# Optimization experiments

Measured on AMD Instinct MI355X. Metric: run time of the kernel, lower is better.

The kernel has to match this reference:

```python
import jax, jax.numpy as jnp
import numpy as np
import math

N_EMBD = 1024
N_HEAD = 16
HEAD_DIM = N_EMBD // N_HEAD
SCALE = 1.0 / math.sqrt(HEAD_DIM)


def setup_inputs() -> dict:
    key = jax.random.key(0)
    ks = jax.random.split(key, 5)
    B, S = 1, 4096
    std = 0.02
    x = jax.random.normal(ks[0], (B, S, N_EMBD), dtype=jnp.float32)
    # Linear weights stored as [in, out] (transposed vs torch storage; same math)
    w_qkv = jax.random.normal(ks[1], (N_EMBD, 3 * N_EMBD), dtype=jnp.float32) * std
    b_qkv = jnp.zeros((3 * N_EMBD,), dtype=jnp.float32)
    w_out = jax.random.normal(ks[2], (N_EMBD, N_EMBD), dtype=jnp.float32) * std
    b_out = jnp.zeros((N_EMBD,), dtype=jnp.float32)
    return {"x": x, "w_qkv": w_qkv, "b_qkv": b_qkv, "w_out": w_out, "b_out": b_out}


def reference(x, w_qkv, b_qkv, w_out, b_out):
    B, S, D = x.shape
    qkv = x @ w_qkv + b_qkv                      # [B, S, 3D]
    q, k, v = jnp.split(qkv, 3, axis=-1)
    # [B, H, S, d]
    q = q.reshape(B, S, N_HEAD, HEAD_DIM).transpose(0, 2, 1, 3)
    k = k.reshape(B, S, N_HEAD, HEAD_DIM).transpose(0, 2, 1, 3)
    v = v.reshape(B, S, N_HEAD, HEAD_DIM).transpose(0, 2, 1, 3)
    scores = jnp.einsum("bhqd,bhkd->bhqk", q, k) * SCALE  # [B, H, S, S]
    causal = jnp.tril(jnp.ones((S, S), dtype=bool))
    scores = jnp.where(causal, scores, -jnp.inf)
    attn = jax.nn.softmax(scores, axis=-1)
    out = jnp.einsum("bhqk,bhkd->bhqd", attn, v)  # [B, H, S, d]
    out = out.transpose(0, 2, 1, 3).reshape(B, S, D)
    return out @ w_out + b_out
```

## Files before the change

### kernel.cpp

```cpp
#include <hip/hip_runtime.h>
#include <hip/hip_bf16.h>
#include <cstdint>

typedef __bf16 bf16x8 __attribute__((ext_vector_type(8)));
typedef float  f32x4  __attribute__((ext_vector_type(4)));

#define S_LEN 4096
#define D_EMB 1024
#define N3    3072
#define HDIM  64

__device__ __forceinline__ unsigned short f2bf(float f) {
    union { unsigned int i; float f; } v; v.f = f;
    unsigned int i = v.i;
    return (unsigned short)((i + 0x7FFFu + ((i >> 16) & 1u)) >> 16);
}

__device__ __forceinline__ void async16(const void* g, void* l) {
    __builtin_amdgcn_global_load_lds(
        (const __attribute__((address_space(1))) unsigned int*)g,
        (__attribute__((address_space(3))) unsigned int*)l,
        16, 0, 0);
}

__global__ void convert_f32_bf16(const float* __restrict__ src,
                                 unsigned short* __restrict__ dst, int n8) {
    const int i = blockIdx.x * blockDim.x + threadIdx.x;
    if (i >= n8) return;
    float4 f0 = *(const float4*)&src[i * 8];
    float4 f1 = *(const float4*)&src[i * 8 + 4];
    union { uint4 q; unsigned short s[8]; } o;
    o.s[0]=f2bf(f0.x); o.s[1]=f2bf(f0.y); o.s[2]=f2bf(f0.z); o.s[3]=f2bf(f0.w);
    o.s[4]=f2bf(f1.x); o.s[5]=f2bf(f1.y); o.s[6]=f2bf(f1.z); o.s[7]=f2bf(f1.w);
    *(uint4*)&dst[i * 8] = o.q;
}

__global__ void transpose_f32_to_bf16(const float* __restrict__ src,
                                      unsigned short* __restrict__ dst,
                                      int R, int ld, int c0) {
    __shared__ float tile[32][33];
    const int tx = threadIdx.x, ty = threadIdx.y;
    const int r0 = blockIdx.y * 32, cc0 = blockIdx.x * 32;
    for (int i = 0; i < 32; i += 8)
        tile[ty + i][tx] = src[(size_t)(r0 + ty + i) * ld + c0 + cc0 + tx];
    __syncthreads();
    for (int i = 0; i < 32; i += 8)
        dst[(size_t)(cc0 + ty + i) * R + r0 + tx] = f2bf(tile[tx][ty + i]);
}

__global__ void transpose_bf16(const unsigned short* __restrict__ src,
                               unsigned short* __restrict__ dst,
                               int R, int ld, int c0) {
    __shared__ unsigned short tile[32][33];
    const int tx = threadIdx.x, ty = threadIdx.y;
    const int r0 = blockIdx.y * 32, cc0 = blockIdx.x * 32;
    for (int i = 0; i < 32; i += 8)
        tile[ty + i][tx] = src[(size_t)(r0 + ty + i) * ld + c0 + cc0 + tx];
    __syncthreads();
    for (int i = 0; i < 32; i += 8)
        dst[(size_t)(cc0 + ty + i) * R + r0 + tx] = tile[tx][ty + i];
}

template <bool OUT_F32>
__global__ __launch_bounds__(256) void gemm_bt_bias(
    const unsigned short* __restrict__ A,
    const unsigned short* __restrict__ BT,
    const float* __restrict__ bias,
    void* __restrict__ Cp,
    int M, int N, int K)
{
    __shared__ __align__(16) unsigned short As[128 * 32];
    __shared__ __align__(16) unsigned short Bs[128 * 32];
    const int tid  = threadIdx.x;
    const int wave = tid >> 6, lane = tid & 63;
    const int q4 = lane >> 4, l16 = lane & 15;
    const int m0 = blockIdx.y * 128, n0 = blockIdx.x * 128;
    const int wm = (wave >> 1) * 64, wn = (wave & 1) * 64;

    f32x4 acc[4][4] = {};

    const int srow = wave * 32 + (lane >> 2);
    const int scol = (lane & 3) * 8;

    for (int k0 = 0; k0 < K; k0 += 32) {
        __syncthreads();
        for (int i = 0; i < 2; ++i) {
            const int r = srow + i * 16;
            async16(A  + (size_t)(m0 + r) * K + k0 + scol,
                    &As[(wave * 32 + i * 16) * 32 + lane * 8]);
            async16(BT + (size_t)(n0 + r) * K + k0 + scol,
                    &Bs[(wave * 32 + i * 16) * 32 + lane * 8]);
        }
        __syncthreads();

        bf16x8 af[4], bfr[4];
        for (int mi = 0; mi < 4; ++mi)
            af[mi] = *(const bf16x8*)&As[(wm + mi * 16 + l16) * 32 + q4 * 8];
        for (int ni = 0; ni < 4; ++ni)
            bfr[ni] = *(const bf16x8*)&Bs[(wn + ni * 16 + l16) * 32 + q4 * 8];
        for (int mi = 0; mi < 4; ++mi)
            for (int ni = 0; ni < 4; ++ni)
                acc[mi][ni] = __builtin_amdgcn_mfma_f32_16x16x32_bf16(
                    af[mi], bfr[ni], acc[mi][ni], 0, 0, 0);
    }

    for (int ni = 0; ni < 4; ++ni) {
        const int col = n0 + wn + ni * 16 + l16;
        const float bv = bias[col];
        for (int mi = 0; mi < 4; ++mi) {
            const int row = m0 + wm + mi * 16 + q4 * 4;
            for (int r = 0; r < 4; ++r) {
                const float val = acc[mi][ni][r] + bv;
                if constexpr (OUT_F32)
                    ((float*)Cp)[(size_t)(row + r) * N + col] = val;
                else
                    ((unsigned short*)Cp)[(size_t)(row + r) * N + col] = f2bf(val);
            }
        }
    }
}

#define LDP 72
__global__ __launch_bounds__(256) void attn_flash(
    const unsigned short* __restrict__ qkv,
    const unsigned short* __restrict__ Vt,
    unsigned short* __restrict__ X2)
{
    __shared__ __align__(16) unsigned short Ks[64 * LDP];
    __shared__ __align__(16) unsigned short Vs[64 * LDP];
    __shared__ __align__(16) unsigned short Ps[4 * 16 * LDP];
    const int tid  = threadIdx.x;
    const int wave = tid >> 6, lane = tid & 63;
    const int q4 = lane >> 4, l16 = lane & 15;
    const int h  = blockIdx.y;

    const int x = blockIdx.x, hg = blockIdx.y >> 2;
    int qt;
    if      (hg == 0) qt = x;
    else if (hg == 1) qt = 63 - x;
    else if (hg == 2) qt = (x + 16) & 63;
    else              qt = (47 - x) & 63;
    const int q0 = qt * 64;

    bf16x8 aq[2];
    {
        const unsigned short* qp =
            qkv + (size_t)(q0 + wave * 16 + l16) * N3 + h * HDIM + q4 * 8;
        aq[0] = *(const bf16x8*)(qp);
        aq[1] = *(const bf16x8*)(qp + 32);
    }

    float l_part = 0.f;
    f32x4 o[4] = {};

    const int rr = tid >> 3;
    const int cc = (tid & 7) * 8;
    const int ntile = qt + 1;
    const int grow = q0 + wave * 16 + l16;

    uint4 kv_a, kv_b, vt_a, vt_b;
    {
        kv_a = *(const uint4*)&qkv[(size_t)(rr)      * N3 + D_EMB + h * HDIM + cc];
        kv_b = *(const uint4*)&qkv[(size_t)(32 + rr) * N3 + D_EMB + h * HDIM + cc];
        vt_a = *(const uint4*)&Vt [(size_t)(h * HDIM + rr)      * S_LEN + cc];
        vt_b = *(const uint4*)&Vt [(size_t)(h * HDIM + 32 + rr) * S_LEN + cc];
    }

    for (int t = 0; t < ntile; ++t) {
        const int kv0 = t * 64;
        __syncthreads();
        *(uint4*)&Ks[rr * LDP + cc]        = kv_a;
        *(uint4*)&Ks[(32 + rr) * LDP + cc] = kv_b;
        *(uint4*)&Vs[rr * LDP + cc]        = vt_a;
        *(uint4*)&Vs[(32 + rr) * LDP + cc] = vt_b;
        if (t + 1 < ntile) {
            const int kn = kv0 + 64;
            kv_a = *(const uint4*)&qkv[(size_t)(kn + rr)      * N3 + D_EMB + h * HDIM + cc];
            kv_b = *(const uint4*)&qkv[(size_t)(kn + 32 + rr) * N3 + D_EMB + h * HDIM + cc];
            vt_a = *(const uint4*)&Vt [(size_t)(h * HDIM + rr)      * S_LEN + kn + cc];
            vt_b = *(const uint4*)&Vt [(size_t)(h * HDIM + 32 + rr) * S_LEN + kn + cc];
        }
        __syncthreads();

        f32x4 sacc[4] = {};
#pragma unroll
        for (int kk = 0; kk < 2; ++kk)
#pragma unroll
            for (int nt = 0; nt < 4; ++nt) {
                bf16x8 kf = *(const bf16x8*)&Ks[(nt * 16 + l16) * LDP + kk * 32 + q4 * 8];
                sacc[nt] = __builtin_amdgcn_mfma_f32_16x16x32_bf16(
                    kf, aq[kk], sacc[nt], 0, 0, 0);
            }

        bf16x8 vb[2][4];
#pragma unroll
        for (int kk = 0; kk < 2; ++kk)
#pragma unroll
            for (int dt = 0; dt < 4; ++dt)
                vb[kk][dt] = *(const bf16x8*)&Vs[(dt * 16 + l16) * LDP + kk * 32 + q4 * 8];

        const bool lastt = (t == ntile - 1);
#pragma unroll
        for (int nt = 0; nt < 4; ++nt) {
            float e[4];
#pragma unroll
            for (int r = 0; r < 4; ++r) {
                e[r] = __expf(sacc[nt][r] * 0.125f);
                if (lastt && (kv0 + nt * 16 + q4 * 4 + r > grow)) e[r] = 0.f;
                l_part += e[r];
            }
            union { uint2 q; unsigned short w[4]; } pk;
            pk.w[0] = f2bf(e[0]); pk.w[1] = f2bf(e[1]);
            pk.w[2] = f2bf(e[2]); pk.w[3] = f2bf(e[3]);
            *(uint2*)&Ps[wave * 16 * LDP + l16 * LDP + nt * 16 + q4 * 4] = pk.q;
        }
        __asm__ volatile("s_waitcnt lgkmcnt(0)" ::: "memory");

#pragma unroll
        for (int kk = 0; kk < 2; ++kk) {
            bf16x8 pa = *(const bf16x8*)&Ps[wave * 16 * LDP + l16 * LDP + kk * 32 + q4 * 8];
#pragma unroll
            for (int dt = 0; dt < 4; ++dt)
                o[dt] = __builtin_amdgcn_mfma_f32_16x16x32_bf16(
                    pa, vb[kk][dt], o[dt], 0, 0, 0);
        }
    }

    float l = l_part;
    l += __shfl_xor(l, 16);
    l += __shfl_xor(l, 32);
    float linv[4];
#pragma unroll
    for (int r = 0; r < 4; ++r)
        linv[r] = 1.f / __shfl(l, q4 * 4 + r);

#pragma unroll
    for (int dt = 0; dt < 4; ++dt)
#pragma unroll
        for (int r = 0; r < 4; ++r) {
            const int row = q0 + wave * 16 + q4 * 4 + r;
            X2[(size_t)row * D_EMB + h * HDIM + dt * 16 + l16] =
                f2bf(o[dt][r] * linv[r]);
        }
}

extern "C" void kernel_launch(void* const* d_in, const int* in_sizes, int n_in,
                              void* d_out, int out_size, void* d_ws, size_t ws_size,
                              hipStream_t stream) {
    const float* x     = (const float*)d_in[0];
    const float* w_qkv = (const float*)d_in[1];
    const float* b_qkv = (const float*)d_in[2];
    const float* w_out = (const float*)d_in[3];
    const float* b_out = (const float*)d_in[4];
    float* out = (float*)d_out;

    char* ws = (char*)d_ws;
    unsigned short* qkv   = (unsigned short*)(ws);
    unsigned short* wqkvT = (unsigned short*)(ws + 25165824);
    unsigned short* woutT = (unsigned short*)(ws + 31457280);
    unsigned short* Vt    = (unsigned short*)(ws + 33554432);
    unsigned short* X2    = (unsigned short*)(ws + 41943040);
    unsigned short* Xb    = X2;

    convert_f32_bf16<<<(4096 * 1024 / 8 + 255) / 256, 256, 0, stream>>>(
        x, Xb, 4096 * 1024 / 8);

    transpose_f32_to_bf16<<<dim3(3072 / 32, 1024 / 32), dim3(32, 8), 0, stream>>>(
        w_qkv, wqkvT, 1024, 3072, 0);
    transpose_f32_to_bf16<<<dim3(1024 / 32, 1024 / 32), dim3(32, 8), 0, stream>>>(
        w_out, woutT, 1024, 1024, 0);

    gemm_bt_bias<false><<<dim3(3072 / 128, 4096 / 128), 256, 0, stream>>>(
        Xb, wqkvT, b_qkv, qkv, 4096, 3072, 1024);

    transpose_bf16<<<dim3(1024 / 32, 4096 / 32), dim3(32, 8), 0, stream>>>(
        qkv, Vt, 4096, 3072, 2048);

    attn_flash<<<dim3(64, 16), 256, 0, stream>>>(qkv, Vt, X2);

    gemm_bt_bias<true><<<dim3(1024 / 128, 4096 / 128), 256, 0, stream>>>(
        X2, woutT, b_out, out, 4096, 1024, 1024);
}
```

Before: 257.9 us.

## Load K fragments directly from global memory and swizzle GEMM block order

The attention kernel stops staging K tiles through shared memory. Each wave now loads its K MFMA fragments straight from global memory, relying on L2/L1 reuse across the four waves, which removes the LDS writes and reads for K. V staging is kept, but V fragments are now read from LDS just before each PV MFMA instead of being preloaded into registers. Separately, the GEMM kernel remaps block indices with an 8-way swizzle to improve L2 locality. The risk is higher global-load latency exposed in the QK stage, since the K loads are no longer prefetched a tile ahead.

```diff
diff --git a/kernel.cpp b/kernel.cpp
--- a/kernel.cpp
+++ b/kernel.cpp
@@ -74,7 +74,11 @@
     const int tid  = threadIdx.x;
     const int wave = tid >> 6, lane = tid & 63;
     const int q4 = lane >> 4, l16 = lane & 15;
-    const int m0 = blockIdx.y * 128, n0 = blockIdx.x * 128;
+
+    const int nwg = gridDim.x * gridDim.y;
+    const int p   = blockIdx.y * gridDim.x + blockIdx.x;
+    const int swz = (p & 7) * (nwg >> 3) + (p >> 3);
+    const int m0 = (swz / gridDim.x) * 128, n0 = (swz % gridDim.x) * 128;
     const int wm = (wave >> 1) * 64, wn = (wave & 1) * 64;
 
     f32x4 acc[4][4] = {};
@@ -126,7 +130,6 @@
     const unsigned short* __restrict__ Vt,
     unsigned short* __restrict__ X2)
 {
-    __shared__ __align__(16) unsigned short Ks[64 * LDP];
     __shared__ __align__(16) unsigned short Vs[64 * LDP];
     __shared__ __align__(16) unsigned short Ps[4 * 16 * LDP];
     const int tid  = threadIdx.x;
@@ -158,46 +161,50 @@
     const int ntile = qt + 1;
     const int grow = q0 + wave * 16 + l16;
 
-    uint4 kv_a, kv_b, vt_a, vt_b;
+    const unsigned short* kfp =
+        qkv + (size_t)l16 * N3 + D_EMB + h * HDIM + q4 * 8;
+
+    uint4 vt_a, vt_b;
     {
-        kv_a = *(const uint4*)&qkv[(size_t)(rr)      * N3 + D_EMB + h * HDIM + cc];
-        kv_b = *(const uint4*)&qkv[(size_t)(32 + rr) * N3 + D_EMB + h * HDIM + cc];
-        vt_a = *(const uint4*)&Vt [(size_t)(h * HDIM + rr)      * S_LEN + cc];
-        vt_b = *(const uint4*)&Vt [(size_t)(h * HDIM + 32 + rr) * S_LEN + cc];
+        vt_a = *(const uint4*)&Vt[(size_t)(h * HDIM + rr)      * S_LEN + cc];
+        vt_b = *(const uint4*)&Vt[(size_t)(h * HDIM + 32 + rr) * S_LEN + cc];
     }
 
     for (int t = 0; t < ntile; ++t) {
         const int kv0 = t * 64;
         __syncthreads();
-        *(uint4*)&Ks[rr * LDP + cc]        = kv_a;
-        *(uint4*)&Ks[(32 + rr) * LDP + cc] = kv_b;
         *(uint4*)&Vs[rr * LDP + cc]        = vt_a;
         *(uint4*)&Vs[(32 + rr) * LDP + cc] = vt_b;
+        __syncthreads();
+
+        f32x4 sacc[4] = {};
+        const unsigned short* kp = kfp + (size_t)kv0 * N3;
+        {
+            bf16x8 kf[4];
+#pragma unroll
+            for (int nt = 0; nt < 4; ++nt)
+                kf[nt] = *(const bf16x8*)(kp + (size_t)nt * 16 * N3);
+#pragma unroll
+            for (int nt = 0; nt < 4; ++nt)
+                sacc[nt] = __builtin_amdgcn_mfma_f32_16x16x32_bf16(
+                    kf[nt], aq[0], sacc[nt], 0, 0, 0);
+        }
+        {
+            bf16x8 kf[4];
+#pragma unroll
+            for (int nt = 0; nt < 4; ++nt)
+                kf[nt] = *(const bf16x8*)(kp + (size_t)nt * 16 * N3 + 32);
+#pragma unroll
+            for (int nt = 0; nt < 4; ++nt)
+                sacc[nt] = __builtin_amdgcn_mfma_f32_16x16x32_bf16(
+                    kf[nt], aq[1], sacc[nt], 0, 0, 0);
+        }
+
         if (t + 1 < ntile) {
             const int kn = kv0 + 64;
-            kv_a = *(const uint4*)&qkv[(size_t)(kn + rr)      * N3 + D_EMB + h * HDIM + cc];
-            kv_b = *(const uint4*)&qkv[(size_t)(kn + 32 + rr) * N3 + D_EMB + h * HDIM + cc];
-            vt_a = *(const uint4*)&Vt [(size_t)(h * HDIM + rr)      * S_LEN + kn + cc];
-            vt_b = *(const uint4*)&Vt [(size_t)(h * HDIM + 32 + rr) * S_LEN + kn + cc];
-        }
-        __syncthreads();
-
-        f32x4 sacc[4] = {};
-#pragma unroll
-        for (int kk = 0; kk < 2; ++kk)
-#pragma unroll
-            for (int nt = 0; nt < 4; ++nt) {
-                bf16x8 kf = *(const bf16x8*)&Ks[(nt * 16 + l16) * LDP + kk * 32 + q4 * 8];
-                sacc[nt] = __builtin_amdgcn_mfma_f32_16x16x32_bf16(
-                    kf, aq[kk], sacc[nt], 0, 0, 0);
-            }
-
-        bf16x8 vb[2][4];
-#pragma unroll
-        for (int kk = 0; kk < 2; ++kk)
-#pragma unroll
-            for (int dt = 0; dt < 4; ++dt)
-                vb[kk][dt] = *(const bf16x8*)&Vs[(dt * 16 + l16) * LDP + kk * 32 + q4 * 8];
+            vt_a = *(const uint4*)&Vt[(size_t)(h * HDIM + rr)      * S_LEN + kn + cc];
+            vt_b = *(const uint4*)&Vt[(size_t)(h * HDIM + 32 + rr) * S_LEN + kn + cc];
+        }
 
         const bool lastt = (t == ntile - 1);
 #pragma unroll
@@ -220,9 +227,11 @@
         for (int kk = 0; kk < 2; ++kk) {
             bf16x8 pa = *(const bf16x8*)&Ps[wave * 16 * LDP + l16 * LDP + kk * 32 + q4 * 8];
 #pragma unroll
-            for (int dt = 0; dt < 4; ++dt)
+            for (int dt = 0; dt < 4; ++dt) {
+                bf16x8 vb = *(const bf16x8*)&Vs[(dt * 16 + l16) * LDP + kk * 32 + q4 * 8];
                 o[dt] = __builtin_amdgcn_mfma_f32_16x16x32_bf16(
-                    pa, vb[kk][dt], o[dt], 0, 0, 0);
+                    pa, vb, o[dt], 0, 0, 0);
+            }
         }
     }
 
```

New measurement: 300.1 us. +16.4%, slower.

## Deepen GEMM K-step to 64, template BM, and stream V fragments in attention

Applied to the files above, without the earlier changes.

The GEMM now stages a 64-wide K slice per barrier pair (two 32-wide LDS buffers), which halves the number of synchronizations per output tile. It is also templated on BM so the output projection uses 64-row tiles, doubling its grid from 256 to 512 blocks to fill more CUs. In the attention kernel, V fragments are loaded from LDS just before each MFMA instead of all up front, which lowers register pressure. The trade-offs are more LDS per block and lower arithmetic intensity on the smaller tiles.

```diff
diff --git a/kernel.cpp b/kernel.cpp
--- a/kernel.cpp
+++ b/kernel.cpp
@@ -61,7 +61,7 @@
         dst[(size_t)(cc0 + ty + i) * R + r0 + tx] = tile[tx][ty + i];
 }
 
-template <bool OUT_F32>
+template <bool OUT_F32, int BM>
 __global__ __launch_bounds__(256) void gemm_bt_bias(
     const unsigned short* __restrict__ A,
     const unsigned short* __restrict__ BT,
@@ -69,46 +69,66 @@
     void* __restrict__ Cp,
     int M, int N, int K)
 {
-    __shared__ __align__(16) unsigned short As[128 * 32];
-    __shared__ __align__(16) unsigned short Bs[128 * 32];
+    constexpr int MI = BM / 32;
+    __shared__ __align__(16) unsigned short As[2][BM * 32];
+    __shared__ __align__(16) unsigned short Bs[2][128 * 32];
     const int tid  = threadIdx.x;
     const int wave = tid >> 6, lane = tid & 63;
     const int q4 = lane >> 4, l16 = lane & 15;
-    const int m0 = blockIdx.y * 128, n0 = blockIdx.x * 128;
-    const int wm = (wave >> 1) * 64, wn = (wave & 1) * 64;
-
-    f32x4 acc[4][4] = {};
-
-    const int srow = wave * 32 + (lane >> 2);
-    const int scol = (lane & 3) * 8;
-
-    for (int k0 = 0; k0 < K; k0 += 32) {
-        __syncthreads();
-        for (int i = 0; i < 2; ++i) {
-            const int r = srow + i * 16;
-            async16(A  + (size_t)(m0 + r) * K + k0 + scol,
-                    &As[(wave * 32 + i * 16) * 32 + lane * 8]);
-            async16(BT + (size_t)(n0 + r) * K + k0 + scol,
-                    &Bs[(wave * 32 + i * 16) * 32 + lane * 8]);
-        }
-        __syncthreads();
-
-        bf16x8 af[4], bfr[4];
-        for (int mi = 0; mi < 4; ++mi)
-            af[mi] = *(const bf16x8*)&As[(wm + mi * 16 + l16) * 32 + q4 * 8];
-        for (int ni = 0; ni < 4; ++ni)
-            bfr[ni] = *(const bf16x8*)&Bs[(wn + ni * 16 + l16) * 32 + q4 * 8];
-        for (int mi = 0; mi < 4; ++mi)
+    const int m0 = blockIdx.y * BM, n0 = blockIdx.x * 128;
+    const int wm = (wave >> 1) * (BM / 2), wn = (wave & 1) * 64;
+
+    f32x4 acc[MI][4] = {};
+
+    const int srowA = wave * (BM / 4) + (lane >> 2);
+    const int srowB = wave * 32 + (lane >> 2);
+    const int scol  = (lane & 3) * 8;
+
+    for (int k0 = 0; k0 < K; k0 += 64) {
+        __syncthreads();
+#pragma unroll
+        for (int kk = 0; kk < 2; ++kk) {
+#pragma unroll
+            for (int i = 0; i < BM / 64; ++i) {
+                const int r = srowA + i * 16;
+                async16(A + (size_t)(m0 + r) * K + k0 + kk * 32 + scol,
+                        &As[kk][(wave * (BM / 4) + i * 16) * 32 + lane * 8]);
+            }
+#pragma unroll
+            for (int i = 0; i < 2; ++i) {
+                const int r = srowB + i * 16;
+                async16(BT + (size_t)(n0 + r) * K + k0 + kk * 32 + scol,
+                        &Bs[kk][(wave * 32 + i * 16) * 32 + lane * 8]);
+            }
+        }
+        __syncthreads();
+
+#pragma unroll
+        for (int kk = 0; kk < 2; ++kk) {
+            bf16x8 af[MI], bfr[4];
+#pragma unroll
+            for (int mi = 0; mi < MI; ++mi)
+                af[mi] = *(const bf16x8*)&As[kk][(wm + mi * 16 + l16) * 32 + q4 * 8];
+#pragma unroll
             for (int ni = 0; ni < 4; ++ni)
-                acc[mi][ni] = __builtin_amdgcn_mfma_f32_16x16x32_bf16(
-                    af[mi], bfr[ni], acc[mi][ni], 0, 0, 0);
-    }
-
+                bfr[ni] = *(const bf16x8*)&Bs[kk][(wn + ni * 16 + l16) * 32 + q4 * 8];
+#pragma unroll
+            for (int mi = 0; mi < MI; ++mi)
+#pragma unroll
+                for (int ni = 0; ni < 4; ++ni)
+                    acc[mi][ni] = __builtin_amdgcn_mfma_f32_16x16x32_bf16(
+                        af[mi], bfr[ni], acc[mi][ni], 0, 0, 0);
+        }
+    }
+
+#pragma unroll
     for (int ni = 0; ni < 4; ++ni) {
         const int col = n0 + wn + ni * 16 + l16;
         const float bv = bias[col];
-        for (int mi = 0; mi < 4; ++mi) {
+#pragma unroll
+        for (int mi = 0; mi < MI; ++mi) {
             const int row = m0 + wm + mi * 16 + q4 * 4;
+#pragma unroll
             for (int r = 0; r < 4; ++r) {
                 const float val = acc[mi][ni][r] + bv;
                 if constexpr (OUT_F32)
@@ -192,13 +212,6 @@
                     kf, aq[kk], sacc[nt], 0, 0, 0);
             }
 
-        bf16x8 vb[2][4];
-#pragma unroll
-        for (int kk = 0; kk < 2; ++kk)
-#pragma unroll
-            for (int dt = 0; dt < 4; ++dt)
-                vb[kk][dt] = *(const bf16x8*)&Vs[(dt * 16 + l16) * LDP + kk * 32 + q4 * 8];
-
         const bool lastt = (t == ntile - 1);
 #pragma unroll
         for (int nt = 0; nt < 4; ++nt) {
@@ -220,9 +233,11 @@
         for (int kk = 0; kk < 2; ++kk) {
             bf16x8 pa = *(const bf16x8*)&Ps[wave * 16 * LDP + l16 * LDP + kk * 32 + q4 * 8];
 #pragma unroll
-            for (int dt = 0; dt < 4; ++dt)
+            for (int dt = 0; dt < 4; ++dt) {
+                bf16x8 vb = *(const bf16x8*)&Vs[(dt * 16 + l16) * LDP + kk * 32 + q4 * 8];
                 o[dt] = __builtin_amdgcn_mfma_f32_16x16x32_bf16(
-                    pa, vb[kk][dt], o[dt], 0, 0, 0);
+                    pa, vb, o[dt], 0, 0, 0);
+            }
         }
     }
 
@@ -270,7 +285,7 @@
     transpose_f32_to_bf16<<<dim3(1024 / 32, 1024 / 32), dim3(32, 8), 0, stream>>>(
         w_out, woutT, 1024, 1024, 0);
 
-    gemm_bt_bias<false><<<dim3(3072 / 128, 4096 / 128), 256, 0, stream>>>(
+    gemm_bt_bias<false, 128><<<dim3(3072 / 128, 4096 / 128), 256, 0, stream>>>(
         Xb, wqkvT, b_qkv, qkv, 4096, 3072, 1024);
 
     transpose_bf16<<<dim3(1024 / 32, 4096 / 32), dim3(32, 8), 0, stream>>>(
@@ -278,6 +293,6 @@
 
     attn_flash<<<dim3(64, 16), 256, 0, stream>>>(qkv, Vt, X2);
 
-    gemm_bt_bias<true><<<dim3(1024 / 128, 4096 / 128), 256, 0, stream>>>(
+    gemm_bt_bias<true, 64><<<dim3(1024 / 128, 4096 / 64), 256, 0, stream>>>(
         X2, woutT, b_out, out, 4096, 1024, 1024);
 }
```

After: 226.6 us. 1.14x faster.
